# Kernel optimization log

Measured on AMD Instinct MI355X. Metric: run time of the kernel, lower is better.

The kernel has to match this reference:

```python
import jax, jax.numpy as jnp
import numpy as np

B, S, H = 2, 2048, 4096
NH, NKV, HD = 32, 8, 128
N_REP = NH // NKV
SCALING = HD ** -0.5


def rotate_half(x):
    x1, x2 = x[..., : HD // 2], x[..., HD // 2 :]
    return jnp.concatenate((-x2, x1), axis=-1)


def setup_inputs() -> dict:
    key = jax.random.key(0)
    ks = jax.random.split(key, 8)
    hidden_states = jax.random.normal(ks[0], (B, S, H), dtype=jnp.float32)
    # RoPE tables computed as in Llama (deterministic, realistic values)
    inv_freq = 1.0 / (10000.0 ** (jnp.arange(0, HD, 2, dtype=jnp.float32) / HD))
    t = jnp.arange(S, dtype=jnp.float32)
    freqs = jnp.einsum('s,d->sd', t, inv_freq)
    emb = jnp.concatenate((freqs, freqs), axis=-1)  # [S, HD]
    cos = jnp.broadcast_to(jnp.cos(emb)[None], (B, S, HD))
    sin = jnp.broadcast_to(jnp.sin(emb)[None], (B, S, HD))
    # additive causal mask [B,1,S,S]
    causal = jnp.where(jnp.tril(jnp.ones((S, S), dtype=bool)), 0.0, -1e9).astype(jnp.float32)
    attention_mask = jnp.broadcast_to(causal[None, None], (B, 1, S, S))
    std = 0.02
    Wq = jax.random.normal(ks[1], (NH * HD, H), dtype=jnp.float32) * std
    Wk = jax.random.normal(ks[2], (NKV * HD, H), dtype=jnp.float32) * std
    Wv = jax.random.normal(ks[3], (NKV * HD, H), dtype=jnp.float32) * std
    Wo = jax.random.normal(ks[4], (H, NH * HD), dtype=jnp.float32) * std
    return dict(hidden_states=hidden_states, cos=cos, sin=sin,
                attention_mask=attention_mask, Wq=Wq, Wk=Wk, Wv=Wv, Wo=Wo)


def reference(hidden_states, cos, sin, attention_mask, Wq, Wk, Wv, Wo):
    b, s, _ = hidden_states.shape
    # projections (torch Linear: x @ W.T), split into heads -> [B, nH, S, HD]
    q = (hidden_states @ Wq.T).reshape(b, s, NH, HD).transpose(0, 2, 1, 3)
    k = (hidden_states @ Wk.T).reshape(b, s, NKV, HD).transpose(0, 2, 1, 3)
    v = (hidden_states @ Wv.T).reshape(b, s, NKV, HD).transpose(0, 2, 1, 3)
    # RoPE: cos/sin [B,S,HD] -> [B,1,S,HD]
    c, sn = cos[:, None], sin[:, None]
    q = q * c + rotate_half(q) * sn
    k = k * c + rotate_half(k) * sn
    # GQA: repeat kv heads
    k = jnp.repeat(k, N_REP, axis=1)
    v = jnp.repeat(v, N_REP, axis=1)
    scores = jnp.einsum('bhqd,bhkd->bhqk', q, k) * SCALING + attention_mask
    attn = jax.nn.softmax(scores.astype(jnp.float32), axis=-1).astype(q.dtype)
    out = jnp.einsum('bhqk,bhkd->bhqd', attn, v)
    out = out.transpose(0, 2, 1, 3).reshape(b, s, NH * HD)
    return out @ Wo.T
```

## Files before the change

### kernel.cpp

```cpp
#include <hip/hip_runtime.h>
#include <stdint.h>

typedef unsigned short u16;
typedef __attribute__((ext_vector_type(8))) short short8;
typedef __attribute__((ext_vector_type(4))) float f32x4;
typedef __attribute__((ext_vector_type(16))) float f32x16;
typedef __attribute__((ext_vector_type(4))) u16 u16x4;

static constexpr float SCALE = 0.08838834764831845f;
static constexpr float QSCALE = 0.12752459769642898f;

__device__ __forceinline__ u16 f2bf(float f) {
    union { float f; unsigned u; } x; x.f = f;
    unsigned r = x.u + 0x7fffu + ((x.u >> 16) & 1u);
    return (u16)(r >> 16);
}
__device__ __forceinline__ float bf2f(u16 b) {
    union { unsigned u; float f; } x; x.u = ((unsigned)b) << 16;
    return x.f;
}
__device__ __forceinline__ unsigned cvt_pk_bf16(float lo, float hi_) {
    unsigned r;
    asm("v_cvt_pk_bf16_f32 %0, %1, %2" : "=v"(r) : "v"(lo), "v"(hi_));
    return r;
}

__global__ __launch_bounds__(256) void convert5_kernel(const float* __restrict__ s0, const float* __restrict__ s1,
                                                       const float* __restrict__ s2, const float* __restrict__ s3,
                                                       const float* __restrict__ s4,
                                                       u16* __restrict__ d0, u16* __restrict__ d1,
                                                       u16* __restrict__ d2, u16* __restrict__ d3,
                                                       u16* __restrict__ d4) {
    const int V0 = 4194304, V1 = 8388608, V2 = 9437184, V3 = 10485760, V4 = 14680064;
    const int stride = gridDim.x * blockDim.x;
    for (int i = blockIdx.x * blockDim.x + threadIdx.x; i < V4; i += stride) {
        const float* sp; u16* dp; int off;
        if (i < V0)      { sp = s0; dp = d0; off = i; }
        else if (i < V1) { sp = s1; dp = d1; off = i - V0; }
        else if (i < V2) { sp = s2; dp = d2; off = i - V1; }
        else if (i < V3) { sp = s3; dp = d3; off = i - V2; }
        else             { sp = s4; dp = d4; off = i - V3; }
        float4 v = *reinterpret_cast<const float4*>(sp + (size_t)off * 4);
        u16x4 o;
        o.x = f2bf(v.x); o.y = f2bf(v.y); o.z = f2bf(v.z); o.w = f2bf(v.w);
        *reinterpret_cast<u16x4*>(dp + (size_t)off * 4) = o;
    }
}

template<int OUT_MODE>
__global__ __launch_bounds__(256) void gemm_bt(const u16* __restrict__ A,
                                               const u16* __restrict__ B,
                                               void* __restrict__ Cv,
                                               int M, int N, int K) {
    constexpr int BK = 64;
    __shared__ u16 sA[128 * BK];
    __shared__ u16 sB[128 * BK];
    const int tid = threadIdx.x;
    const int wid = tid >> 6, lane = tid & 63;
    const int lrow = lane & 15, lgrp = lane >> 4;
    const int row0 = blockIdx.x * 128, col0 = blockIdx.y * 128;
    const int wr = (wid >> 1) * 64, wc = (wid & 1) * 64;

    f32x4 acc[4][4] = {};

    const int NT = K / BK;
    for (int kt = 0; kt < NT; ++kt) {
        const int k0 = kt * BK;
        __syncthreads();
        #pragma unroll
        for (int rnd = 0; rnd < 4; ++rnd) {
            const int eoff = (rnd * 256 + tid) * 8;
            const int r = eoff >> 6, c = eoff & 63;
            const int gc = c ^ ((r & 7) << 3);
            const int ldsoff = rnd * 2048 + wid * 512;
            __builtin_amdgcn_global_load_lds(
                (const __attribute__((address_space(1))) void*)(A + (size_t)(row0 + r) * K + k0 + gc),
                (__attribute__((address_space(3))) void*)(&sA[ldsoff]), 16, 0, 0);
            __builtin_amdgcn_global_load_lds(
                (const __attribute__((address_space(1))) void*)(B + (size_t)(col0 + r) * K + k0 + gc),
                (__attribute__((address_space(3))) void*)(&sB[ldsoff]), 16, 0, 0);
        }
        __syncthreads();
        #pragma unroll
        for (int kk = 0; kk < 2; ++kk) {
            const int koff = kk * 32 + lgrp * 8;
            short8 af[4], bfr[4];
            #pragma unroll
            for (int m = 0; m < 4; ++m) {
                const int rr = wr + m * 16 + lrow;
                af[m] = *(const short8*)&sA[rr * BK + (koff ^ ((rr & 7) << 3))];
            }
            #pragma unroll
            for (int n = 0; n < 4; ++n) {
                const int rr = wc + n * 16 + lrow;
                bfr[n] = *(const short8*)&sB[rr * BK + (koff ^ ((rr & 7) << 3))];
            }
            #pragma unroll
            for (int m = 0; m < 4; ++m)
                #pragma unroll
                for (int n = 0; n < 4; ++n)
                    acc[m][n] = __builtin_amdgcn_mfma_f32_16x16x32_bf16(af[m], bfr[n], acc[m][n], 0, 0, 0);
        }
    }

    const int orow = row0 + wr + lgrp * 4;
    const int ocol = col0 + wc + lrow;
    if (OUT_MODE == 0) {
        u16* C = (u16*)Cv;
        #pragma unroll
        for (int m = 0; m < 4; ++m)
            #pragma unroll
            for (int n = 0; n < 4; ++n)
                #pragma unroll
                for (int r = 0; r < 4; ++r)
                    C[(size_t)(orow + m * 16 + r) * N + ocol + n * 16] = f2bf(acc[m][n][r]);
    } else {
        u16* C = (u16*)Cv;
        #pragma unroll
        for (int m = 0; m < 4; ++m)
            #pragma unroll
            for (int n = 0; n < 4; ++n) {
                u16x4 pk;
                pk.x = f2bf(acc[m][n][0]); pk.y = f2bf(acc[m][n][1]);
                pk.z = f2bf(acc[m][n][2]); pk.w = f2bf(acc[m][n][3]);
                *(u16x4*)&C[(size_t)(ocol + n * 16) * M + orow + m * 16] = pk;
            }
    }
}

template<int OUT_MODE>
__global__ __launch_bounds__(512, 2) void gemm256(const u16* __restrict__ A,
                                                  const u16* __restrict__ B,
                                                  void* __restrict__ Cv,
                                                  int M, int N, int K) {
    __shared__ u16 sA[4][8192];
    __shared__ u16 sB[4][8192];
    const int tid = threadIdx.x;
    const int wid = tid >> 6, lane = tid & 63;
    const int lrow = lane & 15, lgrp = lane >> 4;

    const int nbn = N >> 8;
    const int total = (M >> 8) * nbn;
    int bid = blockIdx.x;
    if ((total & 7) == 0) {
        const int cpx = total >> 3;
        bid = (bid & 7) * cpx + (bid >> 3);
    }
    const int row0 = (bid / nbn) * 256, col0 = (bid % nbn) * 256;
    const int wm = wid >> 2, wn = wid & 3;
    const int wr = wm * 128, wc = wn * 64;

    f32x4 acc[8][4] = {};

    const int rS = wid * 16 + (lane >> 2);
    const int jS = lane & 3;

    auto stageA = [&](int kt) {
        const int s = kt & 3, k0 = kt * 32;
        #pragma unroll
        for (int rd = 0; rd < 2; ++rd) {
            const int r = rd * 128 + rS;
            const int cs = k0 + ((jS ^ ((r >> 1) & 3)) << 3);
            __builtin_amdgcn_global_load_lds(
                (const __attribute__((address_space(1))) void*)(A + (size_t)(row0 + r) * K + cs),
                (__attribute__((address_space(3))) void*)(&sA[s][rd * 4096 + wid * 512]), 16, 0, 0);
        }
    };
    auto stageB = [&](int kt) {
        const int s = kt & 3, k0 = kt * 32;
        #pragma unroll
        for (int rd = 0; rd < 2; ++rd) {
            const int r = rd * 128 + rS;
            const int cs = k0 + ((jS ^ ((r >> 1) & 3)) << 3);
            __builtin_amdgcn_global_load_lds(
                (const __attribute__((address_space(1))) void*)(B + (size_t)(col0 + r) * K + cs),
                (__attribute__((address_space(3))) void*)(&sB[s][rd * 4096 + wid * 512]), 16, 0, 0);
        }
    };

    const int NK = K >> 5;
    stageA(0); stageB(0); stageA(1); stageB(1); stageA(2); stageB(2);
    asm volatile("s_waitcnt vmcnt(8)" ::: "memory");
    __builtin_amdgcn_s_barrier();

    for (int t = 0; t < NK; ++t) {
        const u16* __restrict__ pA = sA[t & 3];
        const u16* __restrict__ pB = sB[t & 3];

        short8 a[4], b[4];
        #pragma unroll
        for (int m = 0; m < 4; ++m) {
            const int ra = wr + m * 16 + lrow;
            a[m] = *(const short8*)&pA[ra * 32 + ((lgrp ^ ((ra >> 1) & 3)) << 3)];
        }
        #pragma unroll
        for (int n = 0; n < 4; ++n) {
            const int rb = wc + n * 16 + lrow;
            b[n] = *(const short8*)&pB[rb * 32 + ((lgrp ^ ((rb >> 1) & 3)) << 3)];
        }
        if (t + 3 < NK) stageA(t + 3);
        __builtin_amdgcn_s_barrier();
        asm volatile("s_waitcnt lgkmcnt(0)" ::: "memory");
        __builtin_amdgcn_sched_barrier(0);
        __builtin_amdgcn_s_setprio(1);
        #pragma unroll
        for (int n = 0; n < 4; ++n)
            #pragma unroll
            for (int m = 0; m < 4; ++m)
                acc[m][n] = __builtin_amdgcn_mfma_f32_16x16x32_bf16(a[m], b[n], acc[m][n], 0, 0, 0);
        __builtin_amdgcn_s_setprio(0);
        __builtin_amdgcn_sched_barrier(0);
        __builtin_amdgcn_s_barrier();

        short8 a2[4];
        #pragma unroll
        for (int m = 0; m < 4; ++m) {
            const int ra = wr + 64 + m * 16 + lrow;
            a2[m] = *(const short8*)&pA[ra * 32 + ((lgrp ^ ((ra >> 1) & 3)) << 3)];
        }
        if (t + 3 < NK) stageB(t + 3);
        __builtin_amdgcn_s_barrier();
        asm volatile("s_waitcnt lgkmcnt(0)" ::: "memory");
        __builtin_amdgcn_sched_barrier(0);
        __builtin_amdgcn_s_setprio(1);
        #pragma unroll
        for (int n = 0; n < 4; ++n)
            #pragma unroll
            for (int m = 0; m < 4; ++m)
                acc[m + 4][n] = __builtin_amdgcn_mfma_f32_16x16x32_bf16(a2[m], b[n], acc[m + 4][n], 0, 0, 0);
        __builtin_amdgcn_s_setprio(0);
        __builtin_amdgcn_sched_barrier(0);
        if (t < NK - 3)       { asm volatile("s_waitcnt vmcnt(8)" ::: "memory"); }
        else if (t == NK - 3) { asm volatile("s_waitcnt vmcnt(4)" ::: "memory"); }
        else if (t == NK - 2) { asm volatile("s_waitcnt vmcnt(0)" ::: "memory"); }
        __builtin_amdgcn_s_barrier();
    }

    const int orow = row0 + wr + lgrp * 4;
    const int ocol = col0 + wc + lrow;
    if (OUT_MODE == 2) {
        float* C = (float*)Cv;
        #pragma unroll
        for (int m = 0; m < 8; ++m)
            #pragma unroll
            for (int n = 0; n < 4; ++n)
                #pragma unroll
                for (int r = 0; r < 4; ++r)
                    C[(size_t)(orow + m * 16 + r) * N + ocol + n * 16] = acc[m][n][r];
    } else {
        u16* C = (u16*)Cv;
        #pragma unroll
        for (int m = 0; m < 8; ++m)
            #pragma unroll
            for (int n = 0; n < 4; ++n)
                #pragma unroll
                for (int r = 0; r < 4; ++r)
                    C[(size_t)(orow + m * 16 + r) * N + ocol + n * 16] = f2bf(acc[m][n][r]);
    }
}

template<int NHEADS>
__global__ __launch_bounds__(256) void rope_kernel(u16* __restrict__ X,
                                                   const float* __restrict__ cosb,
                                                   const float* __restrict__ sinb,
                                                   float scale) {
    constexpr int LH = (NHEADS == 32) ? 5 : 3;
    const int total = 2 * 2048 * NHEADS * 64;
    const int stride = gridDim.x * blockDim.x;
    for (int i = blockIdx.x * blockDim.x + threadIdx.x; i < total; i += stride) {
        const int d = i & 63;
        const int h = (i >> 6) & (NHEADS - 1);
        const int rs = i >> (6 + LH);
        const size_t base = (size_t)rs * (NHEADS * 128) + h * 128 + d;
        const float c = cosb[rs * 128 + d] * scale;
        const float sn = sinb[rs * 128 + d] * scale;
        const float x1 = bf2f(X[base]);
        const float x2 = bf2f(X[base + 64]);
        X[base] = f2bf(x1 * c - x2 * sn);
        X[base + 64] = f2bf(x2 * c + x1 * sn);
    }
}

__global__ __launch_bounds__(512, 2) void attn_kernel(const u16* __restrict__ Q,
                                                      const u16* __restrict__ K,
                                                      const u16* __restrict__ Vt,
                                                      u16* __restrict__ AO) {
    __shared__ u16 sK[2][64 * 128];
    __shared__ u16 sV[2][128 * 64];
    const int tid = threadIdx.x;
    const int wid = tid >> 6, lane = tid & 63;
    const int l31 = lane & 31, hi = lane >> 5;

    const int gg = blockIdx.x >> 6;
    const int bx = (gg < 4) ? gg : 11 - gg;
    const int rem = blockIdx.x & 63;
    const int h = rem >> 1;
    const int b = rem & 1;
    const int hkv = h >> 2;
    const int rs0 = b * 2048;
    const int q0 = bx * 256;
    const int qw = q0 + wid * 32;
    const int q_lane = qw + l31;

    short8 qf[8];
    {
        const u16* qb = Q + (size_t)(rs0 + q_lane) * 4096 + h * 128 + hi * 8;
        #pragma unroll
        for (int f = 0; f < 8; ++f) qf[f] = *(const short8*)(qb + f * 16);
    }

    f32x16 accO[4] = {};
    float m_c = -1e30f, l_c = 0.f;

    auto stage = [&](int bf, int t) {
        const int kv0 = t * 64;
        #pragma unroll
        for (int rnd = 0; rnd < 2; ++rnd) {
            {
                const int e = rnd * 4096 + tid * 8;
                const int r = e >> 7, c = e & 127;
                const int cs = c ^ ((r & 15) << 3);
                __builtin_amdgcn_global_load_lds(
                    (const __attribute__((address_space(1))) void*)(K + (size_t)(rs0 + kv0 + r) * 1024 + hkv * 128 + cs),
                    (__attribute__((address_space(3))) void*)(&sK[bf][rnd * 4096 + wid * 512]), 16, 0, 0);
            }
            {
                const int e = rnd * 4096 + tid * 8;
                const int r = e >> 6, c = e & 63;
                const int cs = c ^ ((r & 7) << 3);
                __builtin_amdgcn_global_load_lds(
                    (const __attribute__((address_space(1))) void*)(Vt + (size_t)(hkv * 128 + r) * 4096 + rs0 + kv0 + cs),
                    (__attribute__((address_space(3))) void*)(&sV[bf][rnd * 4096 + wid * 512]), 16, 0, 0);
            }
        }
    };

    const int NT = 4 * (bx + 1);
    stage(0, 0);
    __syncthreads();
    int buf = 0;

    for (int t = 0; t < NT; ++t) {
        if (t + 1 < NT) stage(buf ^ 1, t + 1);
        const int kv0 = t * 64;

        if (kv0 <= qw + 31) {
            f32x16 sc[2] = {};
            #pragma unroll
            for (int f = 0; f < 8; ++f) {
                const int col = f * 16 + hi * 8;
                const int r0 = l31, r1 = 32 + l31;
                short8 k0 = *(const short8*)&sK[buf][r0 * 128 + (col ^ ((r0 & 15) << 3))];
                short8 k1 = *(const short8*)&sK[buf][r1 * 128 + (col ^ ((r1 & 15) << 3))];
                sc[0] = __builtin_amdgcn_mfma_f32_32x32x16_bf16(k0, qf[f], sc[0], 0, 0, 0);
                sc[1] = __builtin_amdgcn_mfma_f32_32x32x16_bf16(k1, qf[f], sc[1], 0, 0, 0);
            }

            if (kv0 + 63 > q_lane) {
                #pragma unroll
                for (int blk = 0; blk < 2; ++blk)
                    #pragma unroll
                    for (int r = 0; r < 16; ++r) {
                        const int kv_abs = kv0 + blk * 32 + ((r & 3) + 8 * (r >> 2) + 4 * hi);
                        if (kv_abs > q_lane) sc[blk][r] = -1e30f;
                    }
            }

            float mx = sc[0][0];
            #pragma unroll
            for (int blk = 0; blk < 2; ++blk)
                #pragma unroll
                for (int r = 0; r < 16; ++r) mx = fmaxf(mx, sc[blk][r]);
            mx = fmaxf(mx, __shfl_xor(mx, 32));

            if (!__all(mx <= m_c + 8.0f)) {
                const float sclf = __builtin_amdgcn_exp2f(m_c - mx);
                m_c = mx;
                l_c *= sclf;
                float sclq[16];
                #pragma unroll
                for (int r = 0; r < 16; ++r)
                    sclq[r] = __shfl(sclf, (r & 3) + 8 * (r >> 2) + 4 * hi);
                #pragma unroll
                for (int d4 = 0; d4 < 4; ++d4)
                    #pragma unroll
                    for (int r = 0; r < 16; ++r) accO[d4][r] *= sclq[r];
            }
            float ssum = 0.f;
            #pragma unroll
            for (int blk = 0; blk < 2; ++blk)
                #pragma unroll
                for (int r = 0; r < 16; ++r) {
                    const float p = __builtin_amdgcn_exp2f(sc[blk][r] - m_c);
                    sc[blk][r] = p;
                    ssum += p;
                }
            ssum += __shfl_xor(ssum, 32);
            l_c += ssum;

            #pragma unroll
            for (int blk = 0; blk < 2; ++blk) {
                #pragma unroll
                for (int tt = 0; tt < 2; ++tt) {
                    const unsigned cv00 = cvt_pk_bf16(sc[blk][8 * tt + 0], sc[blk][8 * tt + 1]);
                    const unsigned cv01 = cvt_pk_bf16(sc[blk][8 * tt + 2], sc[blk][8 * tt + 3]);
                    const unsigned cv10 = cvt_pk_bf16(sc[blk][8 * tt + 4], sc[blk][8 * tt + 5]);
                    const unsigned cv11 = cvt_pk_bf16(sc[blk][8 * tt + 6], sc[blk][8 * tt + 7]);
                    const unsigned s00 = __shfl_xor(cv00, 32);
                    const unsigned s01 = __shfl_xor(cv01, 32);
                    const unsigned s10 = __shfl_xor(cv10, 32);
                    const unsigned s11 = __shfl_xor(cv11, 32);
                    union { unsigned w[4]; short8 v; } pa;
                    pa.w[0] = hi ? s10 : cv00;
                    pa.w[1] = hi ? s11 : cv01;
                    pa.w[2] = hi ? cv10 : s00;
                    pa.w[3] = hi ? cv11 : s01;
                    const int kvb = blk * 32 + tt * 16 + hi * 8;
                    #pragma unroll
                    for (int d4 = 0; d4 < 4; ++d4) {
                        const int vr = d4 * 32 + l31;
                        short8 vf = *(const short8*)&sV[buf][vr * 64 + (kvb ^ ((vr & 7) << 3))];
                        accO[d4] = __builtin_amdgcn_mfma_f32_32x32x16_bf16(pa.v, vf, accO[d4], 0, 0, 0);
                    }
                }
            }
        }
        __syncthreads();
        buf ^= 1;
    }

    const float invl = 1.0f / l_c;
    float invq[16];
    #pragma unroll
    for (int r = 0; r < 16; ++r)
        invq[r] = __shfl(invl, (r & 3) + 8 * (r >> 2) + 4 * hi);
    #pragma unroll
    for (int d4 = 0; d4 < 4; ++d4)
        #pragma unroll
        for (int r = 0; r < 16; ++r) {
            const int q = qw + (r & 3) + 8 * (r >> 2) + 4 * hi;
            AO[(size_t)(rs0 + q) * 4096 + h * 128 + d4 * 32 + l31] = f2bf(accO[d4][r] * invq[r]);
        }
}

extern "C" void kernel_launch(void* const* d_in, const int* in_sizes, int n_in,
                              void* d_out, int out_size, void* d_ws, size_t ws_size,
                              hipStream_t stream) {
    const float* hs   = (const float*)d_in[0];
    const float* cosp = (const float*)d_in[1];
    const float* sinp = (const float*)d_in[2];
    const float* Wq = (const float*)d_in[4];
    const float* Wk = (const float*)d_in[5];
    const float* Wv = (const float*)d_in[6];
    const float* Wo = (const float*)d_in[7];

    u16* Xb = (u16*)d_out;
    u16* Qb = (u16*)d_out + 16777216;
    char* w = (char*)d_ws;
    u16* Wqb = (u16*)w; w += 33554432;
    u16* Wkb = (u16*)w; w += 8388608;
    u16* Wvb = (u16*)w; w += 8388608;
    u16* Wob = (u16*)w; w += 33554432;
    u16* Kb  = (u16*)w; w += 8388608;
    u16* Vtb = (u16*)w; w += 8388608;
    u16* AOb = (u16*)w; w += 33554432;

    convert5_kernel<<<4096, 256, 0, stream>>>(hs, Wq, Wk, Wv, Wo, Xb, Wqb, Wkb, Wvb, Wob);

    gemm256<0><<<256, 512, 0, stream>>>(Xb, Wqb, Qb, 4096, 4096, 4096);
    gemm_bt<0><<<dim3(32, 8), 256, 0, stream>>>(Xb, Wkb, Kb, 4096, 1024, 4096);
    gemm_bt<1><<<dim3(32, 8), 256, 0, stream>>>(Xb, Wvb, Vtb, 4096, 1024, 4096);

    rope_kernel<32><<<2048, 256, 0, stream>>>(Qb, cosp, sinp, QSCALE);
    rope_kernel<8><<<1024, 256, 0, stream>>>(Kb, cosp, sinp, 1.0f);

    attn_kernel<<<512, 512, 0, stream>>>(Qb, Kb, Vtb, AOb);

    gemm256<2><<<256, 512, 0, stream>>>(AOb, Wob, (float*)d_out, 4096, 4096, 4096);
}
```

Before: 585.2 us.

## Software-pipeline LDS fragment reads across GEMM k-iterations with partial waitcnts

Restructures the GEMM main loop so the next tile's A/B fragments are read from LDS during the second MFMA half of the current iteration, and the a2 fragments are loaded before the first MFMA half. Full lgkmcnt(0) waits and some barriers are replaced with partial lgkmcnt counts, and the vmcnt wait moves between the two halves. The goal is to hide LDS read latency behind MFMA work and cut barrier stalls. It costs extra registers for the prefetched fragments, and the hand-tuned wait counts could introduce races if they are wrong.

```diff
diff --git a/kernel.cpp b/kernel.cpp
--- a/kernel.cpp
+++ b/kernel.cpp
@@ -183,24 +183,31 @@
     asm volatile("s_waitcnt vmcnt(8)" ::: "memory");
     __builtin_amdgcn_s_barrier();
 
+    short8 a[4], b[4];
+    #pragma unroll
+    for (int m = 0; m < 4; ++m) {
+        const int ra = wr + m * 16 + lrow;
+        a[m] = *(const short8*)&sA[0][ra * 32 + ((lgrp ^ ((ra >> 1) & 3)) << 3)];
+    }
+    #pragma unroll
+    for (int n = 0; n < 4; ++n) {
+        const int rb = wc + n * 16 + lrow;
+        b[n] = *(const short8*)&sB[0][rb * 32 + ((lgrp ^ ((rb >> 1) & 3)) << 3)];
+    }
+
     for (int t = 0; t < NK; ++t) {
         const u16* __restrict__ pA = sA[t & 3];
-        const u16* __restrict__ pB = sB[t & 3];
-
-        short8 a[4], b[4];
+        const u16* __restrict__ pAn = sA[(t + 1) & 3];
+        const u16* __restrict__ pBn = sB[(t + 1) & 3];
+
+        short8 a2[4];
         #pragma unroll
         for (int m = 0; m < 4; ++m) {
-            const int ra = wr + m * 16 + lrow;
-            a[m] = *(const short8*)&pA[ra * 32 + ((lgrp ^ ((ra >> 1) & 3)) << 3)];
-        }
-        #pragma unroll
-        for (int n = 0; n < 4; ++n) {
-            const int rb = wc + n * 16 + lrow;
-            b[n] = *(const short8*)&pB[rb * 32 + ((lgrp ^ ((rb >> 1) & 3)) << 3)];
+            const int ra = wr + 64 + m * 16 + lrow;
+            a2[m] = *(const short8*)&pA[ra * 32 + ((lgrp ^ ((ra >> 1) & 3)) << 3)];
         }
         if (t + 3 < NK) stageA(t + 3);
-        __builtin_amdgcn_s_barrier();
-        asm volatile("s_waitcnt lgkmcnt(0)" ::: "memory");
+        asm volatile("s_waitcnt lgkmcnt(4)" ::: "memory");
         __builtin_amdgcn_sched_barrier(0);
         __builtin_amdgcn_s_setprio(1);
         #pragma unroll
@@ -210,17 +217,27 @@
                 acc[m][n] = __builtin_amdgcn_mfma_f32_16x16x32_bf16(a[m], b[n], acc[m][n], 0, 0, 0);
         __builtin_amdgcn_s_setprio(0);
         __builtin_amdgcn_sched_barrier(0);
+        if (t + 3 < NK)       { asm volatile("s_waitcnt vmcnt(6)" ::: "memory"); }
+        else if (t + 3 == NK) { asm volatile("s_waitcnt vmcnt(4)" ::: "memory"); }
+        else if (t + 2 == NK) { asm volatile("s_waitcnt vmcnt(0)" ::: "memory"); }
         __builtin_amdgcn_s_barrier();
 
-        short8 a2[4];
-        #pragma unroll
-        for (int m = 0; m < 4; ++m) {
-            const int ra = wr + 64 + m * 16 + lrow;
-            a2[m] = *(const short8*)&pA[ra * 32 + ((lgrp ^ ((ra >> 1) & 3)) << 3)];
+        short8 na[4], nb[4];
+        if (t + 1 < NK) {
+            #pragma unroll
+            for (int m = 0; m < 4; ++m) {
+                const int ra = wr + m * 16 + lrow;
+                na[m] = *(const short8*)&pAn[ra * 32 + ((lgrp ^ ((ra >> 1) & 3)) << 3)];
+            }
+            #pragma unroll
+            for (int n = 0; n < 4; ++n) {
+                const int rb = wc + n * 16 + lrow;
+                nb[n] = *(const short8*)&pBn[rb * 32 + ((lgrp ^ ((rb >> 1) & 3)) << 3)];
+            }
         }
         if (t + 3 < NK) stageB(t + 3);
-        __builtin_amdgcn_s_barrier();
-        asm volatile("s_waitcnt lgkmcnt(0)" ::: "memory");
+        if (t + 1 < NK) { asm volatile("s_waitcnt lgkmcnt(8)" ::: "memory"); }
+        else            { asm volatile("s_waitcnt lgkmcnt(0)" ::: "memory"); }
         __builtin_amdgcn_sched_barrier(0);
         __builtin_amdgcn_s_setprio(1);
         #pragma unroll
@@ -230,10 +247,10 @@
                 acc[m + 4][n] = __builtin_amdgcn_mfma_f32_16x16x32_bf16(a2[m], b[n], acc[m + 4][n], 0, 0, 0);
         __builtin_amdgcn_s_setprio(0);
         __builtin_amdgcn_sched_barrier(0);
-        if (t < NK - 3)       { asm volatile("s_waitcnt vmcnt(8)" ::: "memory"); }
-        else if (t == NK - 3) { asm volatile("s_waitcnt vmcnt(4)" ::: "memory"); }
-        else if (t == NK - 2) { asm volatile("s_waitcnt vmcnt(0)" ::: "memory"); }
         __builtin_amdgcn_s_barrier();
+
+        #pragma unroll
+        for (int m = 0; m < 4; ++m) { a[m] = na[m]; b[m] = nb[m]; }
     }
 
     const int orow = row0 + wr + lgrp * 4;
```

Result: no change. 588.1 us (+0.5%).

## Restructure 256x256 GEMM into double-buffered BK=64 pipeline with split k-halves

Applied to the files above, without the earlier changes.

Replaces the four-stage BK=32 LDS ring in the 256x256 GEMM with a two-buffer scheme where each buffer holds a BK=64 tile split into two 32-wide halves. The next tile is staged one half at a time between the MFMA groups. The aim is to cut the number of loop iterations and change how global-to-LDS loads overlap with MFMA work. In exchange, prefetch depth drops from three tiles ahead to one, which may expose more memory latency. Each iteration also issues more barriers.

```diff
diff --git a/kernel.cpp b/kernel.cpp
--- a/kernel.cpp
+++ b/kernel.cpp
@@ -129,12 +129,12 @@
 }
 
 template<int OUT_MODE>
-__global__ __launch_bounds__(512, 2) void gemm256(const u16* __restrict__ A,
-                                                  const u16* __restrict__ B,
-                                                  void* __restrict__ Cv,
-                                                  int M, int N, int K) {
-    __shared__ u16 sA[4][8192];
-    __shared__ u16 sB[4][8192];
+__global__ __launch_bounds__(512, 2) void gemm256v2(const u16* __restrict__ A,
+                                                    const u16* __restrict__ B,
+                                                    void* __restrict__ Cv,
+                                                    int M, int N, int K) {
+    __shared__ u16 sA[2][2][256 * 32];
+    __shared__ u16 sB[2][2][256 * 32];
     const int tid = threadIdx.x;
     const int wid = tid >> 6, lane = tid & 63;
     const int lrow = lane & 15, lgrp = lane >> 4;
@@ -142,97 +142,130 @@
     const int nbn = N >> 8;
     const int total = (M >> 8) * nbn;
     int bid = blockIdx.x;
-    if ((total & 7) == 0) {
-        const int cpx = total >> 3;
-        bid = (bid & 7) * cpx + (bid >> 3);
-    }
+    if ((total & 7) == 0) { const int cpx = total >> 3; bid = (bid & 7) * cpx + (bid >> 3); }
     const int row0 = (bid / nbn) * 256, col0 = (bid % nbn) * 256;
-    const int wm = wid >> 2, wn = wid & 3;
-    const int wr = wm * 128, wc = wn * 64;
+    const int wr = (wid >> 2) * 128, wc = (wid & 3) * 64;
 
     f32x4 acc[8][4] = {};
 
-    const int rS = wid * 16 + (lane >> 2);
-    const int jS = lane & 3;
-
-    auto stageA = [&](int kt) {
-        const int s = kt & 3, k0 = kt * 32;
-        #pragma unroll
-        for (int rd = 0; rd < 2; ++rd) {
-            const int r = rd * 128 + rS;
-            const int cs = k0 + ((jS ^ ((r >> 1) & 3)) << 3);
+    const int rS0 = wid * 32 + (lane >> 2);
+    const int uS = lane & 3;
+
+    auto stageA = [&](int nb, int kt, int kkh) {
+        const int k0 = kt * 64 + kkh * 32;
+        #pragma unroll
+        for (int g = 0; g < 2; ++g) {
+            const int r = rS0 + g * 16;
+            const int cs = k0 + ((uS ^ ((r >> 1) & 3)) << 3);
             __builtin_amdgcn_global_load_lds(
                 (const __attribute__((address_space(1))) void*)(A + (size_t)(row0 + r) * K + cs),
-                (__attribute__((address_space(3))) void*)(&sA[s][rd * 4096 + wid * 512]), 16, 0, 0);
+                (__attribute__((address_space(3))) void*)(&sA[nb][kkh][(wid * 32 + g * 16) * 32]), 16, 0, 0);
         }
     };
-    auto stageB = [&](int kt) {
-        const int s = kt & 3, k0 = kt * 32;
-        #pragma unroll
-        for (int rd = 0; rd < 2; ++rd) {
-            const int r = rd * 128 + rS;
-            const int cs = k0 + ((jS ^ ((r >> 1) & 3)) << 3);
+    auto stageB = [&](int nb, int kt, int kkh) {
+        const int k0 = kt * 64 + kkh * 32;
+        #pragma unroll
+        for (int g = 0; g < 2; ++g) {
+            const int r = rS0 + g * 16;
+            const int cs = k0 + ((uS ^ ((r >> 1) & 3)) << 3);
             __builtin_amdgcn_global_load_lds(
                 (const __attribute__((address_space(1))) void*)(B + (size_t)(col0 + r) * K + cs),
-                (__attribute__((address_space(3))) void*)(&sB[s][rd * 4096 + wid * 512]), 16, 0, 0);
+                (__attribute__((address_space(3))) void*)(&sB[nb][kkh][(wid * 32 + g * 16) * 32]), 16, 0, 0);
         }
     };
 
-    const int NK = K >> 5;
-    stageA(0); stageB(0); stageA(1); stageB(1); stageA(2); stageB(2);
-    asm volatile("s_waitcnt vmcnt(8)" ::: "memory");
+    auto rdA = [&](int buf, int kkh, int fr) -> short8 {
+        const int r = wr + fr * 16 + lrow;
+        return *(const short8*)&sA[buf][kkh][r * 32 + ((lgrp ^ ((r >> 1) & 3)) << 3)];
+    };
+    auto rdB = [&](int buf, int kkh, int fc) -> short8 {
+        const int r = wc + fc * 16 + lrow;
+        return *(const short8*)&sB[buf][kkh][r * 32 + ((lgrp ^ ((r >> 1) & 3)) << 3)];
+    };
+
+    const int NK = K >> 6;
+    stageA(0, 0, 0); stageB(0, 0, 0); stageA(0, 0, 1); stageB(0, 0, 1);
+    asm volatile("s_waitcnt vmcnt(4)" ::: "memory");
     __builtin_amdgcn_s_barrier();
 
-    for (int t = 0; t < NK; ++t) {
-        const u16* __restrict__ pA = sA[t & 3];
-        const u16* __restrict__ pB = sB[t & 3];
-
-        short8 a[4], b[4];
-        #pragma unroll
-        for (int m = 0; m < 4; ++m) {
-            const int ra = wr + m * 16 + lrow;
-            a[m] = *(const short8*)&pA[ra * 32 + ((lgrp ^ ((ra >> 1) & 3)) << 3)];
-        }
-        #pragma unroll
-        for (int n = 0; n < 4; ++n) {
-            const int rb = wc + n * 16 + lrow;
-            b[n] = *(const short8*)&pB[rb * 32 + ((lgrp ^ ((rb >> 1) & 3)) << 3)];
-        }
-        if (t + 3 < NK) stageA(t + 3);
+    for (int kt = 0; kt < NK; ++kt) {
+        const int buf = kt & 1, nb = buf ^ 1;
+        const bool st = (kt + 1 < NK);
+        short8 a[4], b[4], a2[4];
+
+        #pragma unroll
+        for (int fr = 0; fr < 4; ++fr) a[fr] = rdA(buf, 0, fr);
+        #pragma unroll
+        for (int fc = 0; fc < 4; ++fc) b[fc] = rdB(buf, 0, fc);
+        if (st) stageA(nb, kt + 1, 0);
+        __builtin_amdgcn_sched_barrier(0);
         __builtin_amdgcn_s_barrier();
         asm volatile("s_waitcnt lgkmcnt(0)" ::: "memory");
         __builtin_amdgcn_sched_barrier(0);
         __builtin_amdgcn_s_setprio(1);
         #pragma unroll
-        for (int n = 0; n < 4; ++n)
-            #pragma unroll
-            for (int m = 0; m < 4; ++m)
-                acc[m][n] = __builtin_amdgcn_mfma_f32_16x16x32_bf16(a[m], b[n], acc[m][n], 0, 0, 0);
+        for (int fr = 0; fr < 4; ++fr)
+            #pragma unroll
+            for (int fc = 0; fc < 4; ++fc)
+                acc[fr][fc] = __builtin_amdgcn_mfma_f32_16x16x32_bf16(a[fr], b[fc], acc[fr][fc], 0, 0, 0);
         __builtin_amdgcn_s_setprio(0);
         __builtin_amdgcn_sched_barrier(0);
         __builtin_amdgcn_s_barrier();
 
-        short8 a2[4];
-        #pragma unroll
-        for (int m = 0; m < 4; ++m) {
-            const int ra = wr + 64 + m * 16 + lrow;
-            a2[m] = *(const short8*)&pA[ra * 32 + ((lgrp ^ ((ra >> 1) & 3)) << 3)];
-        }
-        if (t + 3 < NK) stageB(t + 3);
+        #pragma unroll
+        for (int fr = 0; fr < 4; ++fr) a2[fr] = rdA(buf, 0, fr + 4);
+        if (st) stageB(nb, kt + 1, 0);
+        __builtin_amdgcn_sched_barrier(0);
         __builtin_amdgcn_s_barrier();
         asm volatile("s_waitcnt lgkmcnt(0)" ::: "memory");
         __builtin_amdgcn_sched_barrier(0);
         __builtin_amdgcn_s_setprio(1);
         #pragma unroll
-        for (int n = 0; n < 4; ++n)
-            #pragma unroll
-            for (int m = 0; m < 4; ++m)
-                acc[m + 4][n] = __builtin_amdgcn_mfma_f32_16x16x32_bf16(a2[m], b[n], acc[m + 4][n], 0, 0, 0);
+        for (int fr = 0; fr < 4; ++fr)
+            #pragma unroll
+            for (int fc = 0; fc < 4; ++fc)
+                acc[fr + 4][fc] = __builtin_amdgcn_mfma_f32_16x16x32_bf16(a2[fr], b[fc], acc[fr + 4][fc], 0, 0, 0);
         __builtin_amdgcn_s_setprio(0);
         __builtin_amdgcn_sched_barrier(0);
-        if (t < NK - 3)       { asm volatile("s_waitcnt vmcnt(8)" ::: "memory"); }
-        else if (t == NK - 3) { asm volatile("s_waitcnt vmcnt(4)" ::: "memory"); }
-        else if (t == NK - 2) { asm volatile("s_waitcnt vmcnt(0)" ::: "memory"); }
+        if (st) { asm volatile("s_waitcnt vmcnt(4)" ::: "memory"); }
+        else    { asm volatile("s_waitcnt vmcnt(0)" ::: "memory"); }
+        __builtin_amdgcn_s_barrier();
+
+        #pragma unroll
+        for (int fr = 0; fr < 4; ++fr) a[fr] = rdA(buf, 1, fr);
+        #pragma unroll
+        for (int fc = 0; fc < 4; ++fc) b[fc] = rdB(buf, 1, fc);
+        if (st) stageA(nb, kt + 1, 1);
+        __builtin_amdgcn_sched_barrier(0);
+        __builtin_amdgcn_s_barrier();
+        asm volatile("s_waitcnt lgkmcnt(0)" ::: "memory");
+        __builtin_amdgcn_sched_barrier(0);
+        __builtin_amdgcn_s_setprio(1);
+        #pragma unroll
+        for (int fr = 0; fr < 4; ++fr)
+            #pragma unroll
+            for (int fc = 0; fc < 4; ++fc)
+                acc[fr][fc] = __builtin_amdgcn_mfma_f32_16x16x32_bf16(a[fr], b[fc], acc[fr][fc], 0, 0, 0);
+        __builtin_amdgcn_s_setprio(0);
+        __builtin_amdgcn_sched_barrier(0);
+        __builtin_amdgcn_s_barrier();
+
+        #pragma unroll
+        for (int fr = 0; fr < 4; ++fr) a2[fr] = rdA(buf, 1, fr + 4);
+        if (st) stageB(nb, kt + 1, 1);
+        __builtin_amdgcn_sched_barrier(0);
+        __builtin_amdgcn_s_barrier();
+        asm volatile("s_waitcnt lgkmcnt(0)" ::: "memory");
+        __builtin_amdgcn_sched_barrier(0);
+        __builtin_amdgcn_s_setprio(1);
+        #pragma unroll
+        for (int fr = 0; fr < 4; ++fr)
+            #pragma unroll
+            for (int fc = 0; fc < 4; ++fc)
+                acc[fr + 4][fc] = __builtin_amdgcn_mfma_f32_16x16x32_bf16(a2[fr], b[fc], acc[fr + 4][fc], 0, 0, 0);
+        __builtin_amdgcn_s_setprio(0);
+        __builtin_amdgcn_sched_barrier(0);
+        if (st) { asm volatile("s_waitcnt vmcnt(4)" ::: "memory"); }
         __builtin_amdgcn_s_barrier();
     }
 
@@ -467,7 +500,7 @@
 
     convert5_kernel<<<4096, 256, 0, stream>>>(hs, Wq, Wk, Wv, Wo, Xb, Wqb, Wkb, Wvb, Wob);
 
-    gemm256<0><<<256, 512, 0, stream>>>(Xb, Wqb, Qb, 4096, 4096, 4096);
+    gemm256v2<0><<<256, 512, 0, stream>>>(Xb, Wqb, Qb, 4096, 4096, 4096);
     gemm_bt<0><<<dim3(32, 8), 256, 0, stream>>>(Xb, Wkb, Kb, 4096, 1024, 4096);
     gemm_bt<1><<<dim3(32, 8), 256, 0, stream>>>(Xb, Wvb, Vtb, 4096, 1024, 4096);
 
@@ -476,5 +509,5 @@
 
     attn_kernel<<<512, 512, 0, stream>>>(Qb, Kb, Vtb, AOb);
 
-    gemm256<2><<<256, 512, 0, stream>>>(AOb, Wob, (float*)d_out, 4096, 4096, 4096);
-}
+    gemm256v2<2><<<256, 512, 0, stream>>>(AOb, Wob, (float*)d_out, 4096, 4096, 4096);
+}
```

New measurement: 599.9 us. 1.03x slower.
